# Optimization experiments

Hardware: AMD Instinct MI355X
Metric: run time of the kernel (lower is better)

The kernel has to match this reference:

```python
import jax, jax.numpy as jnp
import numpy as np
from itertools import product

_N = 50000
_G = 52  # voxel grid extent


def _build_maps():
    rs = np.random.RandomState(0)
    ids = rs.choice(_G ** 3, size=_N, replace=False)
    coords = np.stack(np.unravel_index(ids, (_G, _G, _G)), axis=1)  # [N,3]
    order = np.argsort(ids)
    sorted_ids = ids[order]
    in_lists, out_lists = [], []
    for off in product((-1, 0, 1), repeat=3):
        nb = coords + np.array(off)
        valid = np.all((nb >= 0) & (nb < _G), axis=1)
        nb_id = nb[:, 0] * _G * _G + nb[:, 1] * _G + nb[:, 2]
        pos = np.searchsorted(sorted_ids, nb_id)
        pos_c = np.minimum(pos, _N - 1)
        found = valid & (sorted_ids[pos_c] == nb_id)
        in_lists.append(order[pos_c[found]].astype(np.int32))
        out_lists.append(np.nonzero(found)[0].astype(np.int32))
    P = max(len(a) for a in in_lists)  # identity offset -> P == N
    K = len(in_lists)
    in_idx = np.full((K, P), _N, dtype=np.int32)   # sentinel = zero row
    out_idx = np.full((K, P), _N, dtype=np.int32)  # sentinel = dummy out row
    for k in range(K):
        in_idx[k, : len(in_lists[k])] = in_lists[k]
        out_idx[k, : len(out_lists[k])] = out_lists[k]
    pid = (coords[:, 0] // 2) * 26 * 26 + (coords[:, 1] // 2) * 26 + (coords[:, 2] // 2)
    uniq, inv = np.unique(pid, return_inverse=True)
    return in_idx, out_idx, inv.astype(np.int32), int(len(uniq))


def setup_inputs() -> dict:
    key = jax.random.key(0)
    ks = jax.random.split(key, 10)
    in_idx, out_idx, pool_idx, num_pool = _build_maps()
    s1 = 1.0 / np.sqrt(27 * 256)
    s2 = 1.0 / np.sqrt(27 * 512)
    return {
        "feats": jax.random.normal(ks[0], (_N, 256), jnp.float32),
        "W1": jax.random.normal(ks[1], (27, 256, 512), jnp.float32) * s1,
        "g1": 1.0 + 0.1 * jax.random.normal(ks[2], (512,), jnp.float32),
        "b1": 0.05 * jax.random.normal(ks[3], (512,), jnp.float32),
        "W2": jax.random.normal(ks[4], (27, 512, 512), jnp.float32) * s2,
        "g2": 1.0 + 0.1 * jax.random.normal(ks[5], (512,), jnp.float32),
        "b2": 0.05 * jax.random.normal(ks[6], (512,), jnp.float32),
        "W3": jax.random.normal(ks[7], (27, 512, 512), jnp.float32) * s2,
        "g3": 1.0 + 0.1 * jax.random.normal(ks[8], (512,), jnp.float32),
        "b3": 0.05 * jax.random.normal(ks[9], (512,), jnp.float32),
        "in_idx": jnp.asarray(in_idx),
        "out_idx": jnp.asarray(out_idx),
        "pool_idx": jnp.asarray(pool_idx),
        "num_pool": num_pool,
    }


def _sparse_conv(feats, W, in_idx, out_idx):
    # gather-GEMM-scatter over K=27 kernel offsets (MinkowskiConvolution)
    N, Cin = feats.shape
    fp = jnp.concatenate([feats, jnp.zeros((1, Cin), feats.dtype)], axis=0)
    acc0 = jnp.zeros((N + 1, W.shape[-1]), feats.dtype)  # last row = dummy sink
    def step(acc, xs):
        ii, oi, Wk = xs
        return acc.at[oi].add(fp[ii] @ Wk), None
    acc, _ = jax.lax.scan(step, acc0, (in_idx, out_idx, W))
    return acc[:N]


def _bn_relu(x, g, b, eps=1e-5):
    m = x.mean(axis=0)
    v = x.var(axis=0)  # biased, matching torch BN normalization
    return jax.nn.relu((x - m) * jax.lax.rsqrt(v + eps) * g + b)


def reference(feats, W1, g1, b1, W2, g2, b2, W3, g3, b3, in_idx, out_idx, pool_idx, num_pool):
    x = _bn_relu(_sparse_conv(feats, W1, in_idx, out_idx), g1, b1)
    x = _bn_relu(_sparse_conv(x, W2, in_idx, out_idx), g2, b2)
    x = _bn_relu(_sparse_conv(x, W3, in_idx, out_idx), g3, b3)
    return jax.ops.segment_max(x, pool_idx, num_segments=num_pool)
```

## Files before the change

### kernel.cpp

```cpp
#include <hip/hip_runtime.h>
#include <hip/hip_bf16.h>
#include <stdint.h>

typedef __attribute__((ext_vector_type(8))) short bf16x8;
typedef __attribute__((ext_vector_type(4))) float f32x4;
typedef unsigned short u16;

__device__ __forceinline__ u16 f2bf(float x) {
  unsigned u = __float_as_uint(x);
  unsigned r = (u + 0x7FFFu + ((u >> 16) & 1u)) >> 16;
  return (u16)r;
}

__device__ __forceinline__ void gl_lds16(const void* g, void* l) {
  __builtin_amdgcn_global_load_lds((const __attribute__((address_space(1))) void*)g,
                                   (__attribute__((address_space(3))) void*)l, 16, 0, 0);
}


__global__ void zero_f32_kernel(float* p, int n) {
  int i = blockIdx.x * blockDim.x + threadIdx.x;
  if (i < n) p[i] = 0.f;
}

__global__ void init_nbr_kernel(int* nbr, int total, int N) {
  for (int i = blockIdx.x * blockDim.x + threadIdx.x; i < total; i += gridDim.x * blockDim.x)
    nbr[i] = N;
}

__global__ void scatter_nbr_kernel(const int* __restrict__ in_idx, const int* __restrict__ out_idx,
                                   int* __restrict__ nbr, int N, int P, int NPAD) {
  const int total = 27 * P;
  for (int i = blockIdx.x * blockDim.x + threadIdx.x; i < total; i += gridDim.x * blockDim.x) {
    const int o = out_idx[i];
    if ((unsigned)o < (unsigned)N) {
      const int k = i / P;
      nbr[(size_t)k * NPAD + o] = in_idx[i];
    }
  }
}

__global__ void cvt_feats_kernel(const float* __restrict__ F, u16* __restrict__ X0, int N) {
  const int total = (N + 1) * 64;
  for (int i = blockIdx.x * blockDim.x + threadIdx.x; i < total; i += gridDim.x * blockDim.x) {
    const int r = i >> 6;
    ushort4 o;
    if (r < N) {
      const float4 v = ((const float4*)F)[i];
      o.x = f2bf(v.x); o.y = f2bf(v.y); o.z = f2bf(v.z); o.w = f2bf(v.w);
    } else {
      o.x = 0; o.y = 0; o.z = 0; o.w = 0;
    }
    ((ushort4*)X0)[i] = o;
  }
}

__global__ void cvt_w_kernel(const float* __restrict__ W, u16* __restrict__ Wt, int CIN) {
  __shared__ float t[32][33];
  const int k = blockIdx.z;
  const int c0 = blockIdx.y * 32;
  const int n0 = blockIdx.x * 32;
  const int tx = threadIdx.x, ty = threadIdx.y;
  const float* Wk = W + (size_t)k * CIN * 512;
  for (int i = ty; i < 32; i += 8)
    t[i][tx] = Wk[(size_t)(c0 + i) * 512 + n0 + tx];
  __syncthreads();
  u16* Wtk = Wt + (size_t)k * 512 * CIN;
  for (int i = ty; i < 32; i += 8)
    Wtk[(size_t)(n0 + i) * CIN + c0 + tx] = f2bf(t[tx][i]);
}


__global__ void meta_kernel(const int* __restrict__ out_idx, int* __restrict__ meta, int N, int P) {
  __shared__ int sl[27];
  const int k = threadIdx.x;
  if (k < 27) {
    const int* row = out_idx + (size_t)k * P;
    int lo = 0, hi = P;
    while (lo < hi) {
      const int mid = (lo + hi) >> 1;
      if (row[mid] >= N) hi = mid; else lo = mid + 1;
    }
    sl[k] = lo;
  }
  __syncthreads();
  if (threadIdx.x == 0) {
    int zb = 0, ts = 0;
    for (int kk = 0; kk < 27; ++kk) {
      meta[kk] = sl[kk];
      meta[32 + kk] = zb;
      meta[64 + kk] = ts;
      const int tiles = (sl[kk] + 127) >> 7;
      zb += tiles << 7;
      ts += tiles;
    }
    meta[64 + 27] = ts;
    meta[96] = ts;
    meta[97] = zb;
  }
}

__global__ void slots_fill_kernel(int* slots, int total) {
  for (int i = blockIdx.x * blockDim.x + threadIdx.x; i < total; i += gridDim.x * blockDim.x)
    slots[i] = -1;
}

__global__ void scatter_slots_kernel(const int* __restrict__ out_idx, const int* __restrict__ meta,
                                     int* __restrict__ slots, int N, int P, int zrows) {
  const int total = 27 * P;
  for (int i = blockIdx.x * blockDim.x + threadIdx.x; i < total; i += gridDim.x * blockDim.x) {
    const int o = out_idx[i];
    if ((unsigned)o < (unsigned)N) {
      const int k = i / P;
      const int j = i - k * P;
      const int zr = meta[32 + k] + j;
      if (zr < zrows) slots[(size_t)o * 27 + k] = zr;
    }
  }
}


template <int CIN>
__global__ __launch_bounds__(256, 2) void sconv_kernel(
    const u16* __restrict__ X,
    const u16* __restrict__ Wt,
    const int* __restrict__ in_idx,
    const int* __restrict__ meta,
    u16* __restrict__ Z,
    int P, int Nsent, int zrows) {
  constexpr int KK = CIN / 32;
  __shared__ __align__(16) u16 lds[16384];

  const int tid = threadIdx.x;
  const int lane = tid & 63;
  const int wv = tid >> 6;
  const int wm = wv >> 1, wn = wv & 1;
  const int tile = blockIdx.x >> 2;
  const int bn = blockIdx.x & 3;

  const int T = meta[96];
  if (tile >= T) return;
  const int tv = (lane < 28) ? meta[64 + lane] : 0x7fffffff;
  const unsigned long long mk = __ballot(tv <= tile);
  const int k = __popcll(mk) - 1;
  const int ts_k = __shfl(tv, k);
  const int zb = meta[32 + k];
  const int j0 = (tile - ts_k) * 128;
  const int col0 = bn * 128;

  const int sc = tid & 3;
  int srow[2], scs[2];
  size_t boffg[2], arow[2];
  const size_t kb = (size_t)k * 512 * CIN;
#pragma unroll
  for (int i = 0; i < 2; ++i) {
    srow[i] = i * 64 + (tid >> 2);
    scs[i] = (sc ^ ((srow[i] >> 1) & 3)) * 8;
    boffg[i] = kb + (size_t)(col0 + srow[i]) * CIN + scs[i];
    const int j = j0 + srow[i];
    const int idx = (j < P) ? in_idx[(size_t)k * P + j] : Nsent;
    arow[i] = (size_t)idx * CIN;
  }

  const int lr = lane & 15;
  const int q = lane >> 4;
  int aoff[4], boff[4];
#pragma unroll
  for (int f = 0; f < 4; ++f) {
    const int ra = wm * 64 + f * 16 + lr;
    aoff[f] = ra * 32 + ((q ^ ((ra >> 1) & 3)) * 8);
    const int rb = wn * 64 + f * 16 + lr;
    boff[f] = 4096 + rb * 32 + ((q ^ ((rb >> 1) & 3)) * 8);
  }

  f32x4 acc[4][4];
#pragma unroll
  for (int a = 0; a < 4; ++a)
#pragma unroll
    for (int b = 0; b < 4; ++b) acc[a][b] = (f32x4){0.f, 0.f, 0.f, 0.f};

#pragma unroll
  for (int i = 0; i < 2; ++i) {
    gl_lds16(X + arow[i] + scs[i], &lds[i * 2048 + wv * 512]);
    gl_lds16(Wt + boffg[i], &lds[4096 + i * 2048 + wv * 512]);
  }

  int cur = 0;
  for (int s = 0; s < KK; ++s) {
    __syncthreads();
    if (s + 1 < KK) {
      const int nxt = cur ^ 1;
      const int ko = (s + 1) * 32;
#pragma unroll
      for (int i = 0; i < 2; ++i) {
        gl_lds16(X + arow[i] + ko + scs[i], &lds[nxt * 8192 + i * 2048 + wv * 512]);
        gl_lds16(Wt + boffg[i] + ko, &lds[nxt * 8192 + 4096 + i * 2048 + wv * 512]);
      }
    }
    const u16* lb = &lds[cur * 8192];
    bf16x8 av[4], bv[4];
#pragma unroll
    for (int f = 0; f < 4; ++f) av[f] = *(const bf16x8*)&lb[aoff[f]];
#pragma unroll
    for (int f = 0; f < 4; ++f) bv[f] = *(const bf16x8*)&lb[boff[f]];
#pragma unroll
    for (int a = 0; a < 4; ++a)
#pragma unroll
      for (int b = 0; b < 4; ++b)
        acc[a][b] = __builtin_amdgcn_mfma_f32_16x16x32_bf16(av[a], bv[b], acc[a][b], 0, 0, 0);
    cur ^= 1;
  }

#pragma unroll
  for (int a = 0; a < 4; ++a) {
    const int r0 = wm * 64 + a * 16 + q * 4;
#pragma unroll
    for (int b = 0; b < 4; ++b) {
      const int c = col0 + wn * 64 + b * 16 + lr;
#pragma unroll
      for (int j = 0; j < 4; ++j) {
        const int zr = zb + j0 + r0 + j;
        if (zr < zrows) Z[(size_t)zr * 512 + c] = f2bf(acc[a][b][j]);
      }
    }
  }
}


__global__ void gather_bn_kernel(const u16* __restrict__ Z, const int* __restrict__ slots,
                                 float* __restrict__ Y, float* __restrict__ st, int N) {
  __shared__ float ls[1024];
  const int tid = threadIdx.x;
  for (int i = tid; i < 1024; i += 256) ls[i] = 0.f;
  __syncthreads();
  const int lane = tid & 63;
  const int wv = tid >> 6;
  const int nw = gridDim.x * 4;
  const int c0 = lane * 8;
  float s1[8], s2[8];
#pragma unroll
  for (int j = 0; j < 8; ++j) { s1[j] = 0.f; s2[j] = 0.f; }
  for (int o = blockIdx.x * 4 + wv; o < N; o += nw) {
    const int oo = __builtin_amdgcn_readfirstlane(o);
    const int* sl = slots + (size_t)oo * 27;
    float acc[8];
#pragma unroll
    for (int j = 0; j < 8; ++j) acc[j] = 0.f;
#pragma unroll
    for (int k = 0; k < 27; ++k) {
      const int s = sl[k];
      if (s >= 0) {
        const bf16x8 v = *(const bf16x8*)(Z + (size_t)s * 512 + c0);
#pragma unroll
        for (int j = 0; j < 8; ++j)
          acc[j] += __uint_as_float(((unsigned)(u16)v[j]) << 16);
      }
    }
    float4 y0 = {acc[0], acc[1], acc[2], acc[3]};
    float4 y1 = {acc[4], acc[5], acc[6], acc[7]};
    *(float4*)&Y[(size_t)oo * 512 + c0] = y0;
    *(float4*)&Y[(size_t)oo * 512 + c0 + 4] = y1;
#pragma unroll
    for (int j = 0; j < 8; ++j) { s1[j] += acc[j]; s2[j] += acc[j] * acc[j]; }
  }
#pragma unroll
  for (int j = 0; j < 8; ++j) {
    atomicAdd(&ls[c0 + j], s1[j]);
    atomicAdd(&ls[512 + c0 + j], s2[j]);
  }
  __syncthreads();
  for (int i = tid; i < 512; i += 256) {
    atomicAdd(&st[i], ls[i]);
    atomicAdd(&st[512 + i], ls[512 + i]);
  }
}


template <int CIN>
__global__ __launch_bounds__(256, 2) void conv_kernel(
    const u16* __restrict__ X, const u16* __restrict__ Wt, const int* __restrict__ nbr,
    float* __restrict__ Y, int N, int NPAD) {
  constexpr int KK = CIN / 32;
  constexpr int NSTEPS = 27 * KK;
  __shared__ __align__(16) u16 lds[16384];

  const int tid = threadIdx.x;
  const int lane = tid & 63;
  const int wv = tid >> 6;
  const int wm = wv >> 1, wn = wv & 1;
  const int bm = blockIdx.x >> 2;
  const int bn = blockIdx.x & 3;
  const int row0 = bm * 128;
  const int col0 = bn * 128;

  const int sc = tid & 3;
  int srow[2], scs[2];
  size_t boffg[2];
#pragma unroll
  for (int i = 0; i < 2; ++i) {
    srow[i] = i * 64 + (tid >> 2);
    scs[i] = (sc ^ ((srow[i] >> 1) & 3)) * 8;
    boffg[i] = (size_t)(col0 + srow[i]) * CIN + scs[i];
  }

  const int lr = lane & 15;
  const int q = lane >> 4;
  int aoff[4], boff[4];
#pragma unroll
  for (int f = 0; f < 4; ++f) {
    const int ra = wm * 64 + f * 16 + lr;
    aoff[f] = ra * 32 + ((q ^ ((ra >> 1) & 3)) * 8);
    const int rb = wn * 64 + f * 16 + lr;
    boff[f] = 4096 + rb * 32 + ((q ^ ((rb >> 1) & 3)) * 8);
  }

  f32x4 acc[4][4];
#pragma unroll
  for (int a = 0; a < 4; ++a)
#pragma unroll
    for (int b = 0; b < 4; ++b) acc[a][b] = (f32x4){0.f, 0.f, 0.f, 0.f};

  size_t arow[2];
#pragma unroll
  for (int i = 0; i < 2; ++i) arow[i] = (size_t)nbr[row0 + srow[i]] * CIN;

#pragma unroll
  for (int i = 0; i < 2; ++i) {
    gl_lds16(X + arow[i] + scs[i], &lds[i * 2048 + wv * 512]);
    gl_lds16(Wt + boffg[i], &lds[4096 + i * 2048 + wv * 512]);
  }

  int cur = 0;
  for (int s = 0; s < NSTEPS; ++s) {
    __syncthreads();
    const int ns = s + 1;
    if (ns < NSTEPS) {
      const int k = ns / KK;
      const int kk = ns % KK;
      if (kk == 0) {
        const int* nb = nbr + (size_t)k * NPAD + row0;
#pragma unroll
        for (int i = 0; i < 2; ++i) arow[i] = (size_t)nb[srow[i]] * CIN;
      }
      const int nxt = cur ^ 1;
      const int ko = kk * 32;
      const size_t kb = (size_t)k * (512 * CIN);
#pragma unroll
      for (int i = 0; i < 2; ++i) {
        gl_lds16(X + arow[i] + ko + scs[i], &lds[nxt * 8192 + i * 2048 + wv * 512]);
        gl_lds16(Wt + kb + boffg[i] + ko, &lds[nxt * 8192 + 4096 + i * 2048 + wv * 512]);
      }
    }
    const u16* lb = &lds[cur * 8192];
    bf16x8 av[4], bv[4];
#pragma unroll
    for (int f = 0; f < 4; ++f) av[f] = *(const bf16x8*)&lb[aoff[f]];
#pragma unroll
    for (int f = 0; f < 4; ++f) bv[f] = *(const bf16x8*)&lb[boff[f]];
#pragma unroll
    for (int a = 0; a < 4; ++a)
#pragma unroll
      for (int b = 0; b < 4; ++b)
        acc[a][b] = __builtin_amdgcn_mfma_f32_16x16x32_bf16(av[a], bv[b], acc[a][b], 0, 0, 0);
    cur ^= 1;
  }

#pragma unroll
  for (int a = 0; a < 4; ++a) {
    const int r0 = row0 + wm * 64 + a * 16 + q * 4;
#pragma unroll
    for (int b = 0; b < 4; ++b) {
      const int c = col0 + wn * 64 + b * 16 + lr;
#pragma unroll
      for (int j = 0; j < 4; ++j) {
        const int r = r0 + j;
        if (r < N) Y[(size_t)r * 512 + c] = acc[a][b][j];
      }
    }
  }
}

__global__ void bn_stats_kernel(const float* __restrict__ Y, float* __restrict__ st, int N) {
  const int t = threadIdx.x;
  float s0 = 0.f, s1 = 0.f, q0 = 0.f, q1 = 0.f;
  for (int r = blockIdx.x; r < N; r += gridDim.x) {
    const float2 v = *(const float2*)&Y[(size_t)r * 512 + t * 2];
    s0 += v.x; s1 += v.y; q0 += v.x * v.x; q1 += v.y * v.y;
  }
  atomicAdd(&st[2 * t], s0);
  atomicAdd(&st[2 * t + 1], s1);
  atomicAdd(&st[512 + 2 * t], q0);
  atomicAdd(&st[512 + 2 * t + 1], q1);
}

__global__ void bn_finalize_kernel(const float* __restrict__ st, const float* __restrict__ g,
                                   const float* __restrict__ b, float* __restrict__ sc,
                                   float* __restrict__ sh, int N) {
  const int c = threadIdx.x;
  if (c < 512) {
    const float inv = 1.f / (float)N;
    const float m = st[c] * inv;
    const float v = st[512 + c] * inv - m * m;
    const float rs = rsqrtf(v + 1e-5f);
    const float s = rs * g[c];
    sc[c] = s;
    sh[c] = b[c] - m * s;
  }
}

__global__ void bn_norm_kernel(const float* __restrict__ Y, const float* __restrict__ sc,
                               const float* __restrict__ sh, u16* __restrict__ Xn, int N) {
  const int total = (N + 1) * 128;
  for (int i = blockIdx.x * blockDim.x + threadIdx.x; i < total; i += gridDim.x * blockDim.x) {
    const int r = i >> 7;
    const int c = (i & 127) * 4;
    ushort4 o;
    if (r < N) {
      const float4 y = *(const float4*)&Y[(size_t)r * 512 + c];
      const float v0 = fmaxf(fmaf(y.x, sc[c + 0], sh[c + 0]), 0.f);
      const float v1 = fmaxf(fmaf(y.y, sc[c + 1], sh[c + 1]), 0.f);
      const float v2 = fmaxf(fmaf(y.z, sc[c + 2], sh[c + 2]), 0.f);
      const float v3 = fmaxf(fmaf(y.w, sc[c + 3], sh[c + 3]), 0.f);
      o.x = f2bf(v0); o.y = f2bf(v1); o.z = f2bf(v2); o.w = f2bf(v3);
    } else {
      o.x = 0; o.y = 0; o.z = 0; o.w = 0;
    }
    *(ushort4*)&Xn[(size_t)r * 512 + c] = o;
  }
}

__global__ void bn_norm_pool_kernel(const float* __restrict__ Y, const float* __restrict__ sc,
                                    const float* __restrict__ sh, const int* __restrict__ pool,
                                    float* __restrict__ out, int N) {
  const int total = N * 128;
  for (int i = blockIdx.x * blockDim.x + threadIdx.x; i < total; i += gridDim.x * blockDim.x) {
    const int r = i >> 7;
    const int c = (i & 127) * 4;
    const float4 y = *(const float4*)&Y[(size_t)r * 512 + c];
    const int p = pool[r];
    int* ob = (int*)&out[(size_t)p * 512 + c];
    const float v0 = fmaxf(fmaf(y.x, sc[c + 0], sh[c + 0]), 0.f);
    const float v1 = fmaxf(fmaf(y.y, sc[c + 1], sh[c + 1]), 0.f);
    const float v2 = fmaxf(fmaf(y.z, sc[c + 2], sh[c + 2]), 0.f);
    const float v3 = fmaxf(fmaf(y.w, sc[c + 3], sh[c + 3]), 0.f);
    atomicMax(&ob[0], __float_as_int(v0));
    atomicMax(&ob[1], __float_as_int(v1));
    atomicMax(&ob[2], __float_as_int(v2));
    atomicMax(&ob[3], __float_as_int(v3));
  }
}


extern "C" void kernel_launch(void* const* d_in, const int* in_sizes, int n_in,
                              void* d_out, int out_size, void* d_ws, size_t ws_size,
                              hipStream_t stream) {
  const float* feats = (const float*)d_in[0];
  const float* W1 = (const float*)d_in[1];
  const float* g1 = (const float*)d_in[2];
  const float* b1 = (const float*)d_in[3];
  const float* W2 = (const float*)d_in[4];
  const float* g2 = (const float*)d_in[5];
  const float* b2 = (const float*)d_in[6];
  const float* W3 = (const float*)d_in[7];
  const float* g3 = (const float*)d_in[8];
  const float* b3 = (const float*)d_in[9];
  const int* in_idx = (const int*)d_in[10];
  const int* out_idx = (const int*)d_in[11];
  const int* pool_idx = (const int*)d_in[12];
  float* out = (float*)d_out;

  const int N = in_sizes[0] / 256;
  const int P = in_sizes[10] / 27;
  const int NPAD = ((N + 127) / 128) * 128;

  const int ZROWS = 573440;
  const int TILE_CAP = 4480;

  char* w = (char*)d_ws;
  size_t off = 0;
  auto carve = [&](size_t bytes) {
    void* p = w + off;
    off += (bytes + 511) & ~(size_t)511;
    return p;
  };
  u16* X0 = (u16*)carve((size_t)(N + 1) * 256 * 2);
  u16* X1 = (u16*)carve((size_t)(N + 1) * 512 * 2);
  float* Y = (float*)carve((size_t)N * 512 * 4);
  u16* W1t = (u16*)carve((size_t)27 * 512 * 256 * 2);
  u16* W2t = (u16*)carve((size_t)27 * 512 * 512 * 2);
  u16* W3t = (u16*)carve((size_t)27 * 512 * 512 * 2);
  float* st0 = (float*)carve(1024 * 4);
  float* st1 = (float*)carve(1024 * 4);
  float* st2 = (float*)carve(1024 * 4);
  float* sc = (float*)carve(512 * 4);
  float* sh = (float*)carve(512 * 4);
  const size_t common_end = off;

  int* meta = (int*)carve(1024);
  int* slots = (int*)carve((size_t)N * 27 * 4);
  u16* Z = (u16*)carve((size_t)ZROWS * 512 * 2);
  const size_t sparse_need = off;
  const bool use_sparse = (ws_size >= sparse_need);
  (void)n_in; (void)out_size;

  zero_f32_kernel<<<4, 256, 0, stream>>>(st0, 1024);
  zero_f32_kernel<<<4, 256, 0, stream>>>(st1, 1024);
  zero_f32_kernel<<<4, 256, 0, stream>>>(st2, 1024);
  cvt_feats_kernel<<<2048, 256, 0, stream>>>(feats, X0, N);
  cvt_w_kernel<<<dim3(16, 8, 27), dim3(32, 8), 0, stream>>>(W1, W1t, 256);
  cvt_w_kernel<<<dim3(16, 16, 27), dim3(32, 8), 0, stream>>>(W2, W2t, 512);
  cvt_w_kernel<<<dim3(16, 16, 27), dim3(32, 8), 0, stream>>>(W3, W3t, 512);

  if (use_sparse) {
    meta_kernel<<<1, 64, 0, stream>>>(out_idx, meta, N, P);
    slots_fill_kernel<<<1024, 256, 0, stream>>>(slots, 27 * N);
    scatter_slots_kernel<<<1024, 256, 0, stream>>>(out_idx, meta, slots, N, P, ZROWS);
    const int sg = TILE_CAP * 4;

    sconv_kernel<256><<<sg, 256, 0, stream>>>(X0, W1t, in_idx, meta, Z, P, N, ZROWS);
    gather_bn_kernel<<<512, 256, 0, stream>>>(Z, slots, Y, st0, N);
    bn_finalize_kernel<<<1, 512, 0, stream>>>(st0, g1, b1, sc, sh, N);
    bn_norm_kernel<<<4096, 256, 0, stream>>>(Y, sc, sh, X1, N);

    sconv_kernel<512><<<sg, 256, 0, stream>>>(X1, W2t, in_idx, meta, Z, P, N, ZROWS);
    gather_bn_kernel<<<512, 256, 0, stream>>>(Z, slots, Y, st1, N);
    bn_finalize_kernel<<<1, 512, 0, stream>>>(st1, g2, b2, sc, sh, N);
    bn_norm_kernel<<<4096, 256, 0, stream>>>(Y, sc, sh, X1, N);

    sconv_kernel<512><<<sg, 256, 0, stream>>>(X1, W3t, in_idx, meta, Z, P, N, ZROWS);
    gather_bn_kernel<<<512, 256, 0, stream>>>(Z, slots, Y, st2, N);
    bn_finalize_kernel<<<1, 512, 0, stream>>>(st2, g3, b3, sc, sh, N);
    bn_norm_pool_kernel<<<4096, 256, 0, stream>>>(Y, sc, sh, pool_idx, out, N);
  } else {
    int* nbr = (int*)((char*)d_ws + common_end);
    const int convGrid = (NPAD / 128) * 4;
    init_nbr_kernel<<<2048, 256, 0, stream>>>(nbr, 27 * NPAD, N);
    scatter_nbr_kernel<<<2048, 256, 0, stream>>>(in_idx, out_idx, nbr, N, P, NPAD);

    conv_kernel<256><<<convGrid, 256, 0, stream>>>(X0, W1t, nbr, Y, N, NPAD);
    bn_stats_kernel<<<512, 256, 0, stream>>>(Y, st0, N);
    bn_finalize_kernel<<<1, 512, 0, stream>>>(st0, g1, b1, sc, sh, N);
    bn_norm_kernel<<<4096, 256, 0, stream>>>(Y, sc, sh, X1, N);

    conv_kernel<512><<<convGrid, 256, 0, stream>>>(X1, W2t, nbr, Y, N, NPAD);
    bn_stats_kernel<<<512, 256, 0, stream>>>(Y, st1, N);
    bn_finalize_kernel<<<1, 512, 0, stream>>>(st1, g2, b2, sc, sh, N);
    bn_norm_kernel<<<4096, 256, 0, stream>>>(Y, sc, sh, X1, N);

    conv_kernel<512><<<convGrid, 256, 0, stream>>>(X1, W3t, nbr, Y, N, NPAD);
    bn_stats_kernel<<<512, 256, 0, stream>>>(Y, st2, N);
    bn_finalize_kernel<<<1, 512, 0, stream>>>(st2, g3, b3, sc, sh, N);
    bn_norm_pool_kernel<<<4096, 256, 0, stream>>>(Y, sc, sh, pool_idx, out, N);
  }
}
```

Before: 2.176 ms.

## Chunk sparse conv by output rows, handle identity offset as dense GEMM, bf16 Y

```diff
diff --git a/kernel.cpp b/kernel.cpp
--- a/kernel.cpp
+++ b/kernel.cpp
@@ -5,12 +5,22 @@
 typedef __attribute__((ext_vector_type(8))) short bf16x8;
 typedef __attribute__((ext_vector_type(4))) float f32x4;
 typedef unsigned short u16;
+
+#define IDK 13
+
+#define MJLO 64
+#define MKZB 1024
+#define MKTL 2048
+#define MCTL 3072
 
 __device__ __forceinline__ u16 f2bf(float x) {
   unsigned u = __float_as_uint(x);
   unsigned r = (u + 0x7FFFu + ((u >> 16) & 1u)) >> 16;
   return (u16)r;
 }
+__device__ __forceinline__ float bf2f(u16 x) {
+  return __uint_as_float(((unsigned)x) << 16);
+}
 
 __device__ __forceinline__ void gl_lds16(const void* g, void* l) {
   __builtin_amdgcn_global_load_lds((const __attribute__((address_space(1))) void*)g,
@@ -21,23 +31,6 @@
 __global__ void zero_f32_kernel(float* p, int n) {
   int i = blockIdx.x * blockDim.x + threadIdx.x;
   if (i < n) p[i] = 0.f;
-}
-
-__global__ void init_nbr_kernel(int* nbr, int total, int N) {
-  for (int i = blockIdx.x * blockDim.x + threadIdx.x; i < total; i += gridDim.x * blockDim.x)
-    nbr[i] = N;
-}
-
-__global__ void scatter_nbr_kernel(const int* __restrict__ in_idx, const int* __restrict__ out_idx,
-                                   int* __restrict__ nbr, int N, int P, int NPAD) {
-  const int total = 27 * P;
-  for (int i = blockIdx.x * blockDim.x + threadIdx.x; i < total; i += gridDim.x * blockDim.x) {
-    const int o = out_idx[i];
-    if ((unsigned)o < (unsigned)N) {
-      const int k = i / P;
-      nbr[(size_t)k * NPAD + o] = in_idx[i];
-    }
-  }
 }
 
 __global__ void cvt_feats_kernel(const float* __restrict__ F, u16* __restrict__ X0, int N) {
@@ -71,32 +64,51 @@
 }
 
 
-__global__ void meta_kernel(const int* __restrict__ out_idx, int* __restrict__ meta, int N, int P) {
-  __shared__ int sl[27];
-  const int k = threadIdx.x;
-  if (k < 27) {
-    const int* row = out_idx + (size_t)k * P;
+__global__ void meta2_kernel(const int* __restrict__ out_idx, int* __restrict__ meta,
+                             int N, int P, int G, int rpc) {
+  __shared__ int lens[27];
+  const int t = threadIdx.x;
+  if (t < 27) {
+    const int* row = out_idx + (size_t)t * P;
     int lo = 0, hi = P;
     while (lo < hi) {
       const int mid = (lo + hi) >> 1;
       if (row[mid] >= N) hi = mid; else lo = mid + 1;
     }
-    sl[k] = lo;
+    lens[t] = lo;
   }
   __syncthreads();
-  if (threadIdx.x == 0) {
+  const int tot = (G + 1) * 27;
+  for (int idx = t; idx < tot; idx += blockDim.x) {
+    const int c = idx / 27, k = idx - c * 27;
+    const int len = lens[k];
+    int jlo;
+    if (c >= G) {
+      jlo = len;
+    } else {
+      const int target = c * rpc;
+      const int* row = out_idx + (size_t)k * P;
+      int lo = 0, hi = len;
+      while (lo < hi) {
+        const int mid = (lo + hi) >> 1;
+        if (row[mid] < target) lo = mid + 1; else hi = mid;
+      }
+      jlo = lo;
+    }
+    meta[MJLO + c * 32 + k] = jlo;
+  }
+  __syncthreads();
+  if (t < G) {
     int zb = 0, ts = 0;
-    for (int kk = 0; kk < 27; ++kk) {
-      meta[kk] = sl[kk];
-      meta[32 + kk] = zb;
-      meta[64 + kk] = ts;
-      const int tiles = (sl[kk] + 127) >> 7;
+    for (int k = 0; k < 27; ++k) {
+      const int cnt = (k == IDK) ? 0 : (meta[MJLO + (t + 1) * 32 + k] - meta[MJLO + t * 32 + k]);
+      meta[MKZB + t * 32 + k] = zb;
+      meta[MKTL + t * 32 + k] = (k == IDK) ? 0x7fffffff : ts;
+      const int tiles = (cnt + 127) >> 7;
       zb += tiles << 7;
       ts += tiles;
     }
-    meta[64 + 27] = ts;
-    meta[96] = ts;
-    meta[97] = zb;
+    meta[MCTL + t] = ts;
   }
 }
 
@@ -105,29 +117,119 @@
     slots[i] = -1;
 }
 
-__global__ void scatter_slots_kernel(const int* __restrict__ out_idx, const int* __restrict__ meta,
-                                     int* __restrict__ slots, int N, int P, int zrows) {
+__global__ void scatter_slots2_kernel(const int* __restrict__ out_idx, const int* __restrict__ meta,
+                                      int* __restrict__ slots, int N, int P, int rpc, int zcap) {
   const int total = 27 * P;
   for (int i = blockIdx.x * blockDim.x + threadIdx.x; i < total; i += gridDim.x * blockDim.x) {
+    const int k = i / P;
+    if (k == IDK) continue;
     const int o = out_idx[i];
     if ((unsigned)o < (unsigned)N) {
-      const int k = i / P;
       const int j = i - k * P;
-      const int zr = meta[32 + k] + j;
-      if (zr < zrows) slots[(size_t)o * 27 + k] = zr;
+      const int c = o / rpc;
+      const int zr = meta[MKZB + c * 32 + k] + (j - meta[MJLO + c * 32 + k]);
+      if (zr < zcap) slots[(size_t)o * 27 + k] = zr;
     }
   }
 }
 
 
 template <int CIN>
-__global__ __launch_bounds__(256, 2) void sconv_kernel(
-    const u16* __restrict__ X,
-    const u16* __restrict__ Wt,
-    const int* __restrict__ in_idx,
-    const int* __restrict__ meta,
-    u16* __restrict__ Z,
-    int P, int Nsent, int zrows) {
+__global__ __launch_bounds__(256, 2) void ident_kernel(
+    const u16* __restrict__ X, const u16* __restrict__ W13,
+    const int* __restrict__ in13, u16* __restrict__ Y, int N) {
+  constexpr int KK = CIN / 32;
+  __shared__ __align__(16) u16 lds[16384];
+
+  const int tid = threadIdx.x;
+  const int lane = tid & 63;
+  const int wv = tid >> 6;
+  const int wm = wv >> 1, wn = wv & 1;
+  const int row0 = (blockIdx.x >> 2) * 128;
+  const int col0 = (blockIdx.x & 3) * 128;
+
+  const int sc = tid & 3;
+  int srow[2], scs[2];
+  size_t boffg[2], arow[2];
+#pragma unroll
+  for (int i = 0; i < 2; ++i) {
+    srow[i] = i * 64 + (tid >> 2);
+    scs[i] = (sc ^ ((srow[i] >> 1) & 3)) * 8;
+    boffg[i] = (size_t)(col0 + srow[i]) * CIN + scs[i];
+    const int j = row0 + srow[i];
+    const int idx = (j < N) ? in13[j] : N;
+    arow[i] = (size_t)idx * CIN;
+  }
+
+  const int lr = lane & 15;
+  const int q = lane >> 4;
+  int aoff[4], boff[4];
+#pragma unroll
+  for (int f = 0; f < 4; ++f) {
+    const int ra = wm * 64 + f * 16 + lr;
+    aoff[f] = ra * 32 + ((q ^ ((ra >> 1) & 3)) * 8);
+    const int rb = wn * 64 + f * 16 + lr;
+    boff[f] = 4096 + rb * 32 + ((q ^ ((rb >> 1) & 3)) * 8);
+  }
+
+  f32x4 acc[4][4];
+#pragma unroll
+  for (int a = 0; a < 4; ++a)
+#pragma unroll
+    for (int b = 0; b < 4; ++b) acc[a][b] = (f32x4){0.f, 0.f, 0.f, 0.f};
+
+#pragma unroll
+  for (int i = 0; i < 2; ++i) {
+    gl_lds16(X + arow[i] + scs[i], &lds[i * 2048 + wv * 512]);
+    gl_lds16(W13 + boffg[i], &lds[4096 + i * 2048 + wv * 512]);
+  }
+
+  int cur = 0;
+  for (int s = 0; s < KK; ++s) {
+    __syncthreads();
+    if (s + 1 < KK) {
+      const int nxt = cur ^ 1;
+      const int ko = (s + 1) * 32;
+#pragma unroll
+      for (int i = 0; i < 2; ++i) {
+        gl_lds16(X + arow[i] + ko + scs[i], &lds[nxt * 8192 + i * 2048 + wv * 512]);
+        gl_lds16(W13 + boffg[i] + ko, &lds[nxt * 8192 + 4096 + i * 2048 + wv * 512]);
+      }
+    }
+    const u16* lb = &lds[cur * 8192];
+    bf16x8 av[4], bv[4];
+#pragma unroll
+    for (int f = 0; f < 4; ++f) av[f] = *(const bf16x8*)&lb[aoff[f]];
+#pragma unroll
+    for (int f = 0; f < 4; ++f) bv[f] = *(const bf16x8*)&lb[boff[f]];
+#pragma unroll
+    for (int a = 0; a < 4; ++a)
+#pragma unroll
+      for (int b = 0; b < 4; ++b)
+        acc[a][b] = __builtin_amdgcn_mfma_f32_16x16x32_bf16(av[a], bv[b], acc[a][b], 0, 0, 0);
+    cur ^= 1;
+  }
+
+#pragma unroll
+  for (int a = 0; a < 4; ++a) {
+    const int r0 = row0 + wm * 64 + a * 16 + q * 4;
+#pragma unroll
+    for (int b = 0; b < 4; ++b) {
+      const int c = col0 + wn * 64 + b * 16 + lr;
+#pragma unroll
+      for (int j = 0; j < 4; ++j) {
+        const int r = r0 + j;
+        if (r < N) Y[(size_t)r * 512 + c] = f2bf(acc[a][b][j]);
+      }
+    }
+  }
+}
+
+
+template <int CIN>
+__global__ __launch_bounds__(256, 2) void sconv2_kernel(
+    const u16* __restrict__ X, const u16* __restrict__ Wt, const int* __restrict__ in_idx,
+    const int* __restrict__ meta, u16* __restrict__ Z, int P, int Nsent, int zcap, int chunk) {
   constexpr int KK = CIN / 32;
   __shared__ __align__(16) u16 lds[16384];
 
@@ -137,15 +239,17 @@
   const int wm = wv >> 1, wn = wv & 1;
   const int tile = blockIdx.x >> 2;
   const int bn = blockIdx.x & 3;
-
-  const int T = meta[96];
-  if (tile >= T) return;
-  const int tv = (lane < 28) ? meta[64 + lane] : 0x7fffffff;
+  const int c32 = chunk * 32;
+
+  if (tile >= meta[MCTL + chunk]) return;
+  const int tv = (lane < 27) ? meta[MKTL + c32 + lane] : 0x7fffffff;
   const unsigned long long mk = __ballot(tv <= tile);
-  const int k = __popcll(mk) - 1;
-  const int ts_k = __shfl(tv, k);
-  const int zb = meta[32 + k];
-  const int j0 = (tile - ts_k) * 128;
+  const int k = 63 - __builtin_clzll(mk);
+  const int ts_k = meta[MKTL + c32 + k];
+  const int zb = meta[MKZB + c32 + k];
+  const int jlo = meta[MJLO + c32 + k];
+  const int cnt = meta[MJLO + c32 + 32 + k] - jlo;
+  const int local0 = (tile - ts_k) * 128;
   const int col0 = bn * 128;
 
   const int sc = tid & 3;
@@ -157,8 +261,8 @@
     srow[i] = i * 64 + (tid >> 2);
     scs[i] = (sc ^ ((srow[i] >> 1) & 3)) * 8;
     boffg[i] = kb + (size_t)(col0 + srow[i]) * CIN + scs[i];
-    const int j = j0 + srow[i];
-    const int idx = (j < P) ? in_idx[(size_t)k * P + j] : Nsent;
+    const int jl = local0 + srow[i];
+    const int idx = (jl < cnt) ? in_idx[(size_t)k * P + jlo + jl] : Nsent;
     arow[i] = (size_t)idx * CIN;
   }
 
@@ -219,173 +323,50 @@
       const int c = col0 + wn * 64 + b * 16 + lr;
 #pragma unroll
       for (int j = 0; j < 4; ++j) {
-        const int zr = zb + j0 + r0 + j;
-        if (zr < zrows) Z[(size_t)zr * 512 + c] = f2bf(acc[a][b][j]);
-      }
-    }
-  }
-}
-
-
-__global__ void gather_bn_kernel(const u16* __restrict__ Z, const int* __restrict__ slots,
-                                 float* __restrict__ Y, float* __restrict__ st, int N) {
-  __shared__ float ls[1024];
+        const int zr = zb + local0 + r0 + j;
+        if (zr < zcap) Z[(size_t)zr * 512 + c] = f2bf(acc[a][b][j]);
+      }
+    }
+  }
+}
+
+
+__global__ void gather2_kernel(const u16* __restrict__ Z, const int* __restrict__ slots,
+                               u16* __restrict__ Y, int obase, int oend) {
   const int tid = threadIdx.x;
-  for (int i = tid; i < 1024; i += 256) ls[i] = 0.f;
-  __syncthreads();
   const int lane = tid & 63;
   const int wv = tid >> 6;
-  const int nw = gridDim.x * 4;
   const int c0 = lane * 8;
-  float s1[8], s2[8];
-#pragma unroll
-  for (int j = 0; j < 8; ++j) { s1[j] = 0.f; s2[j] = 0.f; }
-  for (int o = blockIdx.x * 4 + wv; o < N; o += nw) {
-    const int oo = __builtin_amdgcn_readfirstlane(o);
-    const int* sl = slots + (size_t)oo * 27;
+  for (int o = obase + blockIdx.x * 4 + wv; o < oend; o += gridDim.x * 4) {
+    const int* sl = slots + (size_t)o * 27;
     float acc[8];
-#pragma unroll
-    for (int j = 0; j < 8; ++j) acc[j] = 0.f;
+    const bf16x8 y0 = *(const bf16x8*)(Y + (size_t)o * 512 + c0);
+#pragma unroll
+    for (int j = 0; j < 8; ++j) acc[j] = bf2f((u16)y0[j]);
 #pragma unroll
     for (int k = 0; k < 27; ++k) {
       const int s = sl[k];
       if (s >= 0) {
         const bf16x8 v = *(const bf16x8*)(Z + (size_t)s * 512 + c0);
 #pragma unroll
-        for (int j = 0; j < 8; ++j)
-          acc[j] += __uint_as_float(((unsigned)(u16)v[j]) << 16);
-      }
-    }
-    float4 y0 = {acc[0], acc[1], acc[2], acc[3]};
-    float4 y1 = {acc[4], acc[5], acc[6], acc[7]};
-    *(float4*)&Y[(size_t)oo * 512 + c0] = y0;
-    *(float4*)&Y[(size_t)oo * 512 + c0 + 4] = y1;
-#pragma unroll
-    for (int j = 0; j < 8; ++j) { s1[j] += acc[j]; s2[j] += acc[j] * acc[j]; }
-  }
-#pragma unroll
-  for (int j = 0; j < 8; ++j) {
-    atomicAdd(&ls[c0 + j], s1[j]);
-    atomicAdd(&ls[512 + c0 + j], s2[j]);
-  }
-  __syncthreads();
-  for (int i = tid; i < 512; i += 256) {
-    atomicAdd(&st[i], ls[i]);
-    atomicAdd(&st[512 + i], ls[512 + i]);
-  }
-}
-
-
-template <int CIN>
-__global__ __launch_bounds__(256, 2) void conv_kernel(
-    const u16* __restrict__ X, const u16* __restrict__ Wt, const int* __restrict__ nbr,
-    float* __restrict__ Y, int N, int NPAD) {
-  constexpr int KK = CIN / 32;
-  constexpr int NSTEPS = 27 * KK;
-  __shared__ __align__(16) u16 lds[16384];
-
-  const int tid = threadIdx.x;
-  const int lane = tid & 63;
-  const int wv = tid >> 6;
-  const int wm = wv >> 1, wn = wv & 1;
-  const int bm = blockIdx.x >> 2;
-  const int bn = blockIdx.x & 3;
-  const int row0 = bm * 128;
-  const int col0 = bn * 128;
-
-  const int sc = tid & 3;
-  int srow[2], scs[2];
-  size_t boffg[2];
-#pragma unroll
-  for (int i = 0; i < 2; ++i) {
-    srow[i] = i * 64 + (tid >> 2);
-    scs[i] = (sc ^ ((srow[i] >> 1) & 3)) * 8;
-    boffg[i] = (size_t)(col0 + srow[i]) * CIN + scs[i];
-  }
-
-  const int lr = lane & 15;
-  const int q = lane >> 4;
-  int aoff[4], boff[4];
-#pragma unroll
-  for (int f = 0; f < 4; ++f) {
-    const int ra = wm * 64 + f * 16 + lr;
-    aoff[f] = ra * 32 + ((q ^ ((ra >> 1) & 3)) * 8);
-    const int rb = wn * 64 + f * 16 + lr;
-    boff[f] = 4096 + rb * 32 + ((q ^ ((rb >> 1) & 3)) * 8);
-  }
-
-  f32x4 acc[4][4];
-#pragma unroll
-  for (int a = 0; a < 4; ++a)
-#pragma unroll
-    for (int b = 0; b < 4; ++b) acc[a][b] = (f32x4){0.f, 0.f, 0.f, 0.f};
-
-  size_t arow[2];
-#pragma unroll
-  for (int i = 0; i < 2; ++i) arow[i] = (size_t)nbr[row0 + srow[i]] * CIN;
-
-#pragma unroll
-  for (int i = 0; i < 2; ++i) {
-    gl_lds16(X + arow[i] + scs[i], &lds[i * 2048 + wv * 512]);
-    gl_lds16(Wt + boffg[i], &lds[4096 + i * 2048 + wv * 512]);
-  }
-
-  int cur = 0;
-  for (int s = 0; s < NSTEPS; ++s) {
-    __syncthreads();
-    const int ns = s + 1;
-    if (ns < NSTEPS) {
-      const int k = ns / KK;
-      const int kk = ns % KK;
-      if (kk == 0) {
-        const int* nb = nbr + (size_t)k * NPAD + row0;
-#pragma unroll
-        for (int i = 0; i < 2; ++i) arow[i] = (size_t)nb[srow[i]] * CIN;
-      }
-      const int nxt = cur ^ 1;
-      const int ko = kk * 32;
-      const size_t kb = (size_t)k * (512 * CIN);
-#pragma unroll
-      for (int i = 0; i < 2; ++i) {
-        gl_lds16(X + arow[i] + ko + scs[i], &lds[nxt * 8192 + i * 2048 + wv * 512]);
-        gl_lds16(Wt + kb + boffg[i] + ko, &lds[nxt * 8192 + 4096 + i * 2048 + wv * 512]);
-      }
-    }
-    const u16* lb = &lds[cur * 8192];
-    bf16x8 av[4], bv[4];
-#pragma unroll
-    for (int f = 0; f < 4; ++f) av[f] = *(const bf16x8*)&lb[aoff[f]];
-#pragma unroll
-    for (int f = 0; f < 4; ++f) bv[f] = *(const bf16x8*)&lb[boff[f]];
-#pragma unroll
-    for (int a = 0; a < 4; ++a)
-#pragma unroll
-      for (int b = 0; b < 4; ++b)
-        acc[a][b] = __builtin_amdgcn_mfma_f32_16x16x32_bf16(av[a], bv[b], acc[a][b], 0, 0, 0);
-    cur ^= 1;
-  }
-
-#pragma unroll
-  for (int a = 0; a < 4; ++a) {
-    const int r0 = row0 + wm * 64 + a * 16 + q * 4;
-#pragma unroll
-    for (int b = 0; b < 4; ++b) {
-      const int c = col0 + wn * 64 + b * 16 + lr;
-#pragma unroll
-      for (int j = 0; j < 4; ++j) {
-        const int r = r0 + j;
-        if (r < N) Y[(size_t)r * 512 + c] = acc[a][b][j];
-      }
-    }
-  }
-}
-
-__global__ void bn_stats_kernel(const float* __restrict__ Y, float* __restrict__ st, int N) {
+        for (int j = 0; j < 8; ++j) acc[j] += bf2f((u16)v[j]);
+      }
+    }
+    bf16x8 outv;
+#pragma unroll
+    for (int j = 0; j < 8; ++j) outv[j] = (short)f2bf(acc[j]);
+    *(bf16x8*)(Y + (size_t)o * 512 + c0) = outv;
+  }
+}
+
+
+__global__ void bn_stats_bf16_kernel(const u16* __restrict__ Y, float* __restrict__ st, int N) {
   const int t = threadIdx.x;
   float s0 = 0.f, s1 = 0.f, q0 = 0.f, q1 = 0.f;
   for (int r = blockIdx.x; r < N; r += gridDim.x) {
-    const float2 v = *(const float2*)&Y[(size_t)r * 512 + t * 2];
-    s0 += v.x; s1 += v.y; q0 += v.x * v.x; q1 += v.y * v.y;
+    const ushort2 v = *(const ushort2*)&Y[(size_t)r * 512 + t * 2];
+    const float a = bf2f(v.x), b = bf2f(v.y);
+    s0 += a; s1 += b; q0 += a * a; q1 += b * b;
   }
   atomicAdd(&st[2 * t], s0);
   atomicAdd(&st[2 * t + 1], s1);
@@ -406,6 +387,179 @@
     sc[c] = s;
     sh[c] = b[c] - m * s;
   }
+}
+
+__global__ void bn_norm_bf16_kernel(const u16* __restrict__ Y, const float* __restrict__ sc,
+                                    const float* __restrict__ sh, u16* __restrict__ Xn, int N) {
+  const int total = (N + 1) * 64;
+  for (int i = blockIdx.x * blockDim.x + threadIdx.x; i < total; i += gridDim.x * blockDim.x) {
+    const int r = i >> 6;
+    const int c = (i & 63) * 8;
+    bf16x8 o;
+    if (r < N) {
+      const bf16x8 y = *(const bf16x8*)&Y[(size_t)r * 512 + c];
+#pragma unroll
+      for (int j = 0; j < 8; ++j) {
+        const float v = fmaxf(fmaf(bf2f((u16)y[j]), sc[c + j], sh[c + j]), 0.f);
+        o[j] = (short)f2bf(v);
+      }
+    } else {
+#pragma unroll
+      for (int j = 0; j < 8; ++j) o[j] = 0;
+    }
+    *(bf16x8*)&Xn[(size_t)r * 512 + c] = o;
+  }
+}
+
+__global__ void bn_norm_pool_bf16_kernel(const u16* __restrict__ Y, const float* __restrict__ sc,
+                                         const float* __restrict__ sh, const int* __restrict__ pool,
+                                         float* __restrict__ out, int N) {
+  const int total = N * 64;
+  for (int i = blockIdx.x * blockDim.x + threadIdx.x; i < total; i += gridDim.x * blockDim.x) {
+    const int r = i >> 6;
+    const int c = (i & 63) * 8;
+    const bf16x8 y = *(const bf16x8*)&Y[(size_t)r * 512 + c];
+    const int p = pool[r];
+    int* ob = (int*)&out[(size_t)p * 512 + c];
+#pragma unroll
+    for (int j = 0; j < 8; ++j) {
+      const float v = fmaxf(fmaf(bf2f((u16)y[j]), sc[c + j], sh[c + j]), 0.f);
+      atomicMax(&ob[j], __float_as_int(v));
+    }
+  }
+}
+
+
+__global__ void init_nbr_kernel(int* nbr, int total, int N) {
+  for (int i = blockIdx.x * blockDim.x + threadIdx.x; i < total; i += gridDim.x * blockDim.x)
+    nbr[i] = N;
+}
+
+__global__ void scatter_nbr_kernel(const int* __restrict__ in_idx, const int* __restrict__ out_idx,
+                                   int* __restrict__ nbr, int N, int P, int NPAD) {
+  const int total = 27 * P;
+  for (int i = blockIdx.x * blockDim.x + threadIdx.x; i < total; i += gridDim.x * blockDim.x) {
+    const int o = out_idx[i];
+    if ((unsigned)o < (unsigned)N) {
+      const int k = i / P;
+      nbr[(size_t)k * NPAD + o] = in_idx[i];
+    }
+  }
+}
+
+template <int CIN>
+__global__ __launch_bounds__(256, 2) void conv_kernel(
+    const u16* __restrict__ X, const u16* __restrict__ Wt, const int* __restrict__ nbr,
+    float* __restrict__ Y, int N, int NPAD) {
+  constexpr int KK = CIN / 32;
+  constexpr int NSTEPS = 27 * KK;
+  __shared__ __align__(16) u16 lds[16384];
+
+  const int tid = threadIdx.x;
+  const int lane = tid & 63;
+  const int wv = tid >> 6;
+  const int wm = wv >> 1, wn = wv & 1;
+  const int row0 = (blockIdx.x >> 2) * 128;
+  const int col0 = (blockIdx.x & 3) * 128;
+
+  const int sc = tid & 3;
+  int srow[2], scs[2];
+  size_t boffg[2];
+#pragma unroll
+  for (int i = 0; i < 2; ++i) {
+    srow[i] = i * 64 + (tid >> 2);
+    scs[i] = (sc ^ ((srow[i] >> 1) & 3)) * 8;
+    boffg[i] = (size_t)(col0 + srow[i]) * CIN + scs[i];
+  }
+
+  const int lr = lane & 15;
+  const int q = lane >> 4;
+  int aoff[4], boff[4];
+#pragma unroll
+  for (int f = 0; f < 4; ++f) {
+    const int ra = wm * 64 + f * 16 + lr;
+    aoff[f] = ra * 32 + ((q ^ ((ra >> 1) & 3)) * 8);
+    const int rb = wn * 64 + f * 16 + lr;
+    boff[f] = 4096 + rb * 32 + ((q ^ ((rb >> 1) & 3)) * 8);
+  }
+
+  f32x4 acc[4][4];
+#pragma unroll
+  for (int a = 0; a < 4; ++a)
+#pragma unroll
+    for (int b = 0; b < 4; ++b) acc[a][b] = (f32x4){0.f, 0.f, 0.f, 0.f};
+
+  size_t arow[2];
+#pragma unroll
+  for (int i = 0; i < 2; ++i) arow[i] = (size_t)nbr[row0 + srow[i]] * CIN;
+
+#pragma unroll
+  for (int i = 0; i < 2; ++i) {
+    gl_lds16(X + arow[i] + scs[i], &lds[i * 2048 + wv * 512]);
+    gl_lds16(Wt + boffg[i], &lds[4096 + i * 2048 + wv * 512]);
+  }
+
+  int cur = 0;
+  for (int s = 0; s < NSTEPS; ++s) {
+    __syncthreads();
+    const int ns = s + 1;
+    if (ns < NSTEPS) {
+      const int k = ns / KK;
+      const int kk = ns % KK;
+      if (kk == 0) {
+        const int* nb = nbr + (size_t)k * NPAD + row0;
+#pragma unroll
+        for (int i = 0; i < 2; ++i) arow[i] = (size_t)nb[srow[i]] * CIN;
+      }
+      const int nxt = cur ^ 1;
+      const int ko = kk * 32;
+      const size_t kb = (size_t)k * (512 * CIN);
+#pragma unroll
+      for (int i = 0; i < 2; ++i) {
+        gl_lds16(X + arow[i] + ko + scs[i], &lds[nxt * 8192 + i * 2048 + wv * 512]);
+        gl_lds16(Wt + kb + boffg[i] + ko, &lds[nxt * 8192 + 4096 + i * 2048 + wv * 512]);
+      }
+    }
+    const u16* lb = &lds[cur * 8192];
+    bf16x8 av[4], bv[4];
+#pragma unroll
+    for (int f = 0; f < 4; ++f) av[f] = *(const bf16x8*)&lb[aoff[f]];
+#pragma unroll
+    for (int f = 0; f < 4; ++f) bv[f] = *(const bf16x8*)&lb[boff[f]];
+#pragma unroll
+    for (int a = 0; a < 4; ++a)
+#pragma unroll
+      for (int b = 0; b < 4; ++b)
+        acc[a][b] = __builtin_amdgcn_mfma_f32_16x16x32_bf16(av[a], bv[b], acc[a][b], 0, 0, 0);
+    cur ^= 1;
+  }
+
+#pragma unroll
+  for (int a = 0; a < 4; ++a) {
+    const int r0 = row0 + wm * 64 + a * 16 + q * 4;
+#pragma unroll
+    for (int b = 0; b < 4; ++b) {
+      const int c = col0 + wn * 64 + b * 16 + lr;
+#pragma unroll
+      for (int j = 0; j < 4; ++j) {
+        const int r = r0 + j;
+        if (r < N) Y[(size_t)r * 512 + c] = acc[a][b][j];
+      }
+    }
+  }
+}
+
+__global__ void bn_stats_kernel(const float* __restrict__ Y, float* __restrict__ st, int N) {
+  const int t = threadIdx.x;
+  float s0 = 0.f, s1 = 0.f, q0 = 0.f, q1 = 0.f;
+  for (int r = blockIdx.x; r < N; r += gridDim.x) {
+    const float2 v = *(const float2*)&Y[(size_t)r * 512 + t * 2];
+    s0 += v.x; s1 += v.y; q0 += v.x * v.x; q1 += v.y * v.y;
+  }
+  atomicAdd(&st[2 * t], s0);
+  atomicAdd(&st[2 * t + 1], s1);
+  atomicAdd(&st[512 + 2 * t], q0);
+  atomicAdd(&st[512 + 2 * t + 1], q1);
 }
 
 __global__ void bn_norm_kernel(const float* __restrict__ Y, const float* __restrict__ sc,
@@ -472,9 +626,7 @@
   const int N = in_sizes[0] / 256;
   const int P = in_sizes[10] / 27;
   const int NPAD = ((N + 127) / 128) * 128;
-
-  const int ZROWS = 573440;
-  const int TILE_CAP = 4480;
+  (void)n_in; (void)out_size;
 
   char* w = (char*)d_ws;
   size_t off = 0;
@@ -483,9 +635,10 @@
     off += (bytes + 511) & ~(size_t)511;
     return p;
   };
+
   u16* X0 = (u16*)carve((size_t)(N + 1) * 256 * 2);
   u16* X1 = (u16*)carve((size_t)(N + 1) * 512 * 2);
-  float* Y = (float*)carve((size_t)N * 512 * 4);
+  u16* Yb = (u16*)carve((size_t)N * 512 * 2);
   u16* W1t = (u16*)carve((size_t)27 * 512 * 256 * 2);
   u16* W2t = (u16*)carve((size_t)27 * 512 * 512 * 2);
   u16* W3t = (u16*)carve((size_t)27 * 512 * 512 * 2);
@@ -494,62 +647,109 @@
   float* st2 = (float*)carve(1024 * 4);
   float* sc = (float*)carve(512 * 4);
   float* sh = (float*)carve(512 * 4);
-  const size_t common_end = off;
-
-  int* meta = (int*)carve(1024);
+  int* meta = (int*)carve(16384);
   int* slots = (int*)carve((size_t)N * 27 * 4);
-  u16* Z = (u16*)carve((size_t)ZROWS * 512 * 2);
-  const size_t sparse_need = off;
-  const bool use_sparse = (ws_size >= sparse_need);
-  (void)n_in; (void)out_size;
-
-  zero_f32_kernel<<<4, 256, 0, stream>>>(st0, 1024);
-  zero_f32_kernel<<<4, 256, 0, stream>>>(st1, 1024);
-  zero_f32_kernel<<<4, 256, 0, stream>>>(st2, 1024);
-  cvt_feats_kernel<<<2048, 256, 0, stream>>>(feats, X0, N);
-  cvt_w_kernel<<<dim3(16, 8, 27), dim3(32, 8), 0, stream>>>(W1, W1t, 256);
-  cvt_w_kernel<<<dim3(16, 16, 27), dim3(32, 8), 0, stream>>>(W2, W2t, 512);
-  cvt_w_kernel<<<dim3(16, 16, 27), dim3(32, 8), 0, stream>>>(W3, W3t, 512);
+  const size_t sparse_base = off;
+  u16* Z = (u16*)(w + sparse_base);
+
+  const long long UPPER = 490000;
+  const long long avail = (ws_size > sparse_base) ? (long long)(ws_size - sparse_base) : 0;
+  const long long zcap_rows_ll = avail / 1024;
+  const int usable = (int)((zcap_rows_ll > 6144) ? (zcap_rows_ll - 6144) : 0);
+  const bool use_sparse = (usable >= 20500);
 
   if (use_sparse) {
-    meta_kernel<<<1, 64, 0, stream>>>(out_idx, meta, N, P);
+    const int G = (int)((UPPER + usable - 1) / usable);
+    const int rpc = (N + G - 1) / G;
+    const int zcap = (int)((zcap_rows_ll < 600000) ? zcap_rows_ll : 600000);
+    const long long tb = UPPER / G + 6144;
+    const int tcap = (int)(((zcap_rows_ll < tb) ? zcap_rows_ll : tb) >> 7) + 1;
+    const int sgrid = tcap * 4;
+    const int ggrid = ((rpc + 3) / 4 < 8192) ? (rpc + 3) / 4 : 8192;
+    const int igrid = (NPAD / 128) * 4;
+
+    zero_f32_kernel<<<4, 256, 0, stream>>>(st0, 1024);
+    zero_f32_kernel<<<4, 256, 0, stream>>>(st1, 1024);
+    zero_f32_kernel<<<4, 256, 0, stream>>>(st2, 1024);
+    cvt_feats_kernel<<<2048, 256, 0, stream>>>(feats, X0, N);
+    cvt_w_kernel<<<dim3(16, 8, 27), dim3(32, 8), 0, stream>>>(W1, W1t, 256);
+    cvt_w_kernel<<<dim3(16, 16, 27), dim3(32, 8), 0, stream>>>(W2, W2t, 512);
+    cvt_w_kernel<<<dim3(16, 16, 27), dim3(32, 8), 0, stream>>>(W3, W3t, 512);
+    meta2_kernel<<<1, 1024, 0, stream>>>(out_idx, meta, N, P, G, rpc);
     slots_fill_kernel<<<1024, 256, 0, stream>>>(slots, 27 * N);
-    scatter_slots_kernel<<<1024, 256, 0, stream>>>(out_idx, meta, slots, N, P, ZROWS);
-    const int sg = TILE_CAP * 4;
-
-    sconv_kernel<256><<<sg, 256, 0, stream>>>(X0, W1t, in_idx, meta, Z, P, N, ZROWS);
-    gather_bn_kernel<<<512, 256, 0, stream>>>(Z, slots, Y, st0, N);
+    scatter_slots2_kernel<<<2048, 256, 0, stream>>>(out_idx, meta, slots, N, P, rpc, zcap);
+
+    ident_kernel<256><<<igrid, 256, 0, stream>>>(X0, W1t + (size_t)IDK * 512 * 256,
+                                                 in_idx + (size_t)IDK * P, Yb, N);
+    for (int c = 0; c < G; ++c) {
+      const int oend = ((c + 1) * rpc < N) ? (c + 1) * rpc : N;
+      sconv2_kernel<256><<<sgrid, 256, 0, stream>>>(X0, W1t, in_idx, meta, Z, P, N, zcap, c);
+      gather2_kernel<<<ggrid, 256, 0, stream>>>(Z, slots, Yb, c * rpc, oend);
+    }
+    bn_stats_bf16_kernel<<<512, 256, 0, stream>>>(Yb, st0, N);
     bn_finalize_kernel<<<1, 512, 0, stream>>>(st0, g1, b1, sc, sh, N);
-    bn_norm_kernel<<<4096, 256, 0, stream>>>(Y, sc, sh, X1, N);
-
-    sconv_kernel<512><<<sg, 256, 0, stream>>>(X1, W2t, in_idx, meta, Z, P, N, ZROWS);
-    gather_bn_kernel<<<512, 256, 0, stream>>>(Z, slots, Y, st1, N);
+    bn_norm_bf16_kernel<<<4096, 256, 0, stream>>>(Yb, sc, sh, X1, N);
+
+    ident_kernel<512><<<igrid, 256, 0, stream>>>(X1, W2t + (size_t)IDK * 512 * 512,
+                                                 in_idx + (size_t)IDK * P, Yb, N);
+    for (int c = 0; c < G; ++c) {
+      const int oend = ((c + 1) * rpc < N) ? (c + 1) * rpc : N;
+      sconv2_kernel<512><<<sgrid, 256, 0, stream>>>(X1, W2t, in_idx, meta, Z, P, N, zcap, c);
+      gather2_kernel<<<ggrid, 256, 0, stream>>>(Z, slots, Yb, c * rpc, oend);
+    }
+    bn_stats_bf16_kernel<<<512, 256, 0, stream>>>(Yb, st1, N);
     bn_finalize_kernel<<<1, 512, 0, stream>>>(st1, g2, b2, sc, sh, N);
-    bn_norm_kernel<<<4096, 256, 0, stream>>>(Y, sc, sh, X1, N);
-
-    sconv_kernel<512><<<sg, 256, 0, stream>>>(X1, W3t, in_idx, meta, Z, P, N, ZROWS);
-    gather_bn_kernel<<<512, 256, 0, stream>>>(Z, slots, Y, st2, N);
+    bn_norm_bf16_kernel<<<4096, 256, 0, stream>>>(Yb, sc, sh, X1, N);
+
+    ident_kernel<512><<<igrid, 256, 0, stream>>>(X1, W3t + (size_t)IDK * 512 * 512,
+                                                 in_idx + (size_t)IDK * P, Yb, N);
+    for (int c = 0; c < G; ++c) {
+      const int oend = ((c + 1) * rpc < N) ? (c + 1) * rpc : N;
+      sconv2_kernel<512><<<sgrid, 256, 0, stream>>>(X1, W3t, in_idx, meta, Z, P, N, zcap, c);
+      gather2_kernel<<<ggrid, 256, 0, stream>>>(Z, slots, Yb, c * rpc, oend);
+    }
+    bn_stats_bf16_kernel<<<512, 256, 0, stream>>>(Yb, st2, N);
     bn_finalize_kernel<<<1, 512, 0, stream>>>(st2, g3, b3, sc, sh, N);
-    bn_norm_pool_kernel<<<4096, 256, 0, stream>>>(Y, sc, sh, pool_idx, out, N);
+    bn_norm_pool_bf16_kernel<<<4096, 256, 0, stream>>>(Yb, sc, sh, pool_idx, out, N);
   } else {
-    int* nbr = (int*)((char*)d_ws + common_end);
+    off = 0;
+    u16* dX0 = (u16*)carve((size_t)(N + 1) * 256 * 2);
+    u16* dX1 = (u16*)carve((size_t)(N + 1) * 512 * 2);
+    float* dY = (float*)carve((size_t)N * 512 * 4);
+    u16* dW1t = (u16*)carve((size_t)27 * 512 * 256 * 2);
+    u16* dW2t = (u16*)carve((size_t)27 * 512 * 512 * 2);
+    u16* dW3t = (u16*)carve((size_t)27 * 512 * 512 * 2);
+    float* dst0 = (float*)carve(1024 * 4);
+    float* dst1 = (float*)carve(1024 * 4);
+    float* dst2 = (float*)carve(1024 * 4);
+    float* dsc = (float*)carve(512 * 4);
+    float* dsh = (float*)carve(512 * 4);
+    int* nbr = (int*)carve((size_t)27 * NPAD * 4);
     const int convGrid = (NPAD / 128) * 4;
+
+    zero_f32_kernel<<<4, 256, 0, stream>>>(dst0, 1024);
+    zero_f32_kernel<<<4, 256, 0, stream>>>(dst1, 1024);
+    zero_f32_kernel<<<4, 256, 0, stream>>>(dst2, 1024);
+    cvt_feats_kernel<<<2048, 256, 0, stream>>>(feats, dX0, N);
+    cvt_w_kernel<<<dim3(16, 8, 27), dim3(32, 8), 0, stream>>>(W1, dW1t, 256);
+    cvt_w_kernel<<<dim3(16, 16, 27), dim3(32, 8), 0, stream>>>(W2, dW2t, 512);
+    cvt_w_kernel<<<dim3(16, 16, 27), dim3(32, 8), 0, stream>>>(W3, dW3t, 512);
     init_nbr_kernel<<<2048, 256, 0, stream>>>(nbr, 27 * NPAD, N);
     scatter_nbr_kernel<<<2048, 256, 0, stream>>>(in_idx, out_idx, nbr, N, P, NPAD);
 
-    conv_kernel<256><<<convGrid, 256, 0, stream>>>(X0, W1t, nbr, Y, N, NPAD);
-    bn_stats_kernel<<<512, 256, 0, stream>>>(Y, st0, N);
-    bn_finalize_kernel<<<1, 512, 0, stream>>>(st0, g1, b1, sc, sh, N);
-    bn_norm_kernel<<<4096, 256, 0, stream>>>(Y, sc, sh, X1, N);
-
-    conv_kernel<512><<<convGrid, 256, 0, stream>>>(X1, W2t, nbr, Y, N, NPAD);
-    bn_stats_kernel<<<512, 256, 0, stream>>>(Y, st1, N);
-    bn_finalize_kernel<<<1, 512, 0, stream>>>(st1, g2, b2, sc, sh, N);
-    bn_norm_kernel<<<4096, 256, 0, stream>>>(Y, sc, sh, X1, N);
-
-    conv_kernel<512><<<convGrid, 256, 0, stream>>>(X1, W3t, nbr, Y, N, NPAD);
-    bn_stats_kernel<<<512, 256, 0, stream>>>(Y, st2, N);
-    bn_finalize_kernel<<<1, 512, 0, stream>>>(st2, g3, b3, sc, sh, N);
-    bn_norm_pool_kernel<<<4096, 256, 0, stream>>>(Y, sc, sh, pool_idx, out, N);
-  }
-}
+    conv_kernel<256><<<convGrid, 256, 0, stream>>>(dX0, dW1t, nbr, dY, N, NPAD);
+    bn_stats_kernel<<<512, 256, 0, stream>>>(dY, dst0, N);
+    bn_finalize_kernel<<<1, 512, 0, stream>>>(dst0, g1, b1, dsc, dsh, N);
+    bn_norm_kernel<<<4096, 256, 0, stream>>>(dY, dsc, dsh, dX1, N);
+
+    conv_kernel<512><<<convGrid, 256, 0, stream>>>(dX1, dW2t, nbr, dY, N, NPAD);
+    bn_stats_kernel<<<512, 256, 0, stream>>>(dY, dst1, N);
+    bn_finalize_kernel<<<1, 512, 0, stream>>>(dst1, g2, b2, dsc, dsh, N);
+    bn_norm_kernel<<<4096, 256, 0, stream>>>(dY, dsc, dsh, dX1, N);
+
+    conv_kernel<512><<<convGrid, 256, 0, stream>>>(dX1, dW3t, nbr, dY, N, NPAD);
+    bn_stats_kernel<<<512, 256, 0, stream>>>(dY, dst2, N);
+    bn_finalize_kernel<<<1, 512, 0, stream>>>(dst2, g3, b3, dsc, dsh, N);
+    bn_norm_pool_kernel<<<4096, 256, 0, stream>>>(dY, dsc, dsh, pool_idx, out, N);
+  }
+}
```

After: 2.436 ms. 12.0% more time.
